# Performance work log

Measured on AMD Instinct MI355X. Metric: run time of the kernel, lower is better.

Reference implementation:

```python
import jax, jax.numpy as jnp
import numpy as np

BIG = 1e9
EPS_BETA = 1e-6
EPS_BN = 1e-5

N_NODES = 50000
N_EDGES = 800000
IN_DIM = 128
OUT_DIM = 128


def setup_inputs() -> dict:
    key = jax.random.key(0)
    ks = jax.random.split(key, 8)
    h = jax.random.normal(ks[0], (N_NODES, IN_DIM), dtype=jnp.float32)
    src = jax.random.randint(ks[1], (N_EDGES,), 0, N_NODES, dtype=jnp.int32)
    dst = jax.random.randint(ks[2], (N_EDGES,), 0, N_NODES, dtype=jnp.int32)
    sigma_GD = jax.random.uniform(ks[3], (N_EDGES,), dtype=jnp.float32)
    fc_w = jax.random.normal(ks[4], (IN_DIM, OUT_DIM), dtype=jnp.float32) / np.sqrt(IN_DIM)
    fc_b = jax.random.normal(ks[5], (OUT_DIM,), dtype=jnp.float32) * 0.01
    attn_w = jax.random.normal(ks[6], (2 * OUT_DIM, 1), dtype=jnp.float32) / np.sqrt(2 * OUT_DIM)
    attn_b = jax.random.normal(ks[7], (1,), dtype=jnp.float32) * 0.01
    bn_gamma = jnp.ones((OUT_DIM,), dtype=jnp.float32)
    bn_beta = jnp.zeros((OUT_DIM,), dtype=jnp.float32)
    return {"h": h, "src": src, "dst": dst, "sigma_GD": sigma_GD,
            "fc_w": fc_w, "fc_b": fc_b, "attn_w": attn_w, "attn_b": attn_b,
            "bn_gamma": bn_gamma, "bn_beta": bn_beta}


def reference(h, src, dst, sigma_GD, fc_w, fc_b, attn_w, attn_b, bn_gamma, bn_beta):
    n = h.shape[0]
    # node projection
    z = h @ fc_w + fc_b                                   # [N, D]
    z = jnp.where(jnp.isinf(z), BIG, z)
    # per-edge attention logits: concat(src,dst) @ W == src@W1 + dst@W2 (avoid concat materialization)
    d = z.shape[1]
    w_src, w_dst = attn_w[:d], attn_w[d:]
    z_src = z[src]                                        # [E, D]
    a = z_src @ w_src + z[dst] @ w_dst + attn_b           # [E, 1]
    a = jnp.where(jnp.isinf(a), BIG, a)
    e = jax.nn.leaky_relu(a, negative_slope=0.01)[:, 0]   # [E]
    # segment softmax over incoming edges (mailbox softmax)
    m = jax.ops.segment_max(e, dst, num_segments=n)       # [N]
    ex = jnp.exp(e - m[dst])
    denom = jax.ops.segment_sum(ex, dst, num_segments=n)  # [N]
    alpha = ex / denom[dst]                               # [E]
    # beta: sigma_GD normalized per destination node
    bsum = jax.ops.segment_sum(sigma_GD, dst, num_segments=n)
    beta = sigma_GD / (bsum[dst] + EPS_BETA)              # [E]
    # weighted scatter-sum of source features
    h_new = jax.ops.segment_sum((alpha * beta)[:, None] * z_src, dst, num_segments=n)  # [N, D]
    h_new = jnp.where(jnp.isinf(h_new), BIG, h_new)
    # BatchNorm1d (training-mode batch stats, biased variance, as torch does)
    mu = h_new.mean(axis=0)
    var = ((h_new - mu) ** 2).mean(axis=0)
    h_bn = (h_new - mu) * jax.lax.rsqrt(var + EPS_BN) * bn_gamma + bn_beta
    return jax.nn.elu(h_bn)
```

## Files before the change

kernel.cpp:

```cpp
#include <hip/hip_runtime.h>
#include <hip/hip_fp16.h>
#include <math.h>

#define N_NODES 50000
#define N_EDGES 800000
#define BIGV 1000000000.0f
#define NBLK_SCAN 196
#define NBLK_GEMM 3125

typedef _Float16 half8 __attribute__((ext_vector_type(8)));
typedef float floatx4 __attribute__((ext_vector_type(4)));

__device__ __forceinline__ float clampinf(float x) { return isinf(x) ? BIGV : x; }

__device__ __forceinline__ void barrier_lgkm_only() {
    __builtin_amdgcn_sched_barrier(0);
    asm volatile("s_waitcnt lgkmcnt(0)" ::: "memory");
    __builtin_amdgcn_s_barrier();
    __builtin_amdgcn_sched_barrier(0);
}

__global__ __launch_bounds__(256) void k_wcast(const float* __restrict__ W,
                                               __half* __restrict__ wt,
                                               int* __restrict__ cursor,
                                               float* __restrict__ bns)
{
    int idx = blockIdx.x * 256 + threadIdx.x;
    int n = idx >> 7, k = idx & 127;
    wt[idx] = __float2half(W[k * 128 + n]);
    for (int i = idx; i < N_NODES; i += 16384) cursor[i] = 0;
    if (idx < 256) bns[idx] = 0.f;
}

__global__ __launch_bounds__(256) void k_gemm(
    const float* __restrict__ h, const __half* __restrict__ wt,
    const float* __restrict__ bias, const float* __restrict__ attn_w,
    const int* __restrict__ dst, __half* __restrict__ zh,
    float* __restrict__ sv, float* __restrict__ tv,
    int* __restrict__ cursor, int* __restrict__ rank)
{
    __shared__ _Float16 hA[16][136];
    __shared__ float spart[4][16], tpart[4][16];

    const int tid = threadIdx.x;
    const int lane = tid & 63;
    const int wv = tid >> 6;
    const int l16 = lane & 15;
    const int oct = lane >> 4;
    const int n0 = wv << 5;
    const int node0 = blockIdx.x << 4;

    const int e = blockIdx.x * 256 + tid;
    const int d = dst[e];

    {
        const float4* h4 = (const float4*)(h + (size_t)node0 * 128);
        for (int i = tid; i < 512; i += 256) {
            int r = i >> 5, c4 = i & 31;
            float4 v = h4[i];
            union { __half2 h2[2]; uint2 u; } pk;
            pk.h2[0] = __floats2half2_rn(v.x, v.y);
            pk.h2[1] = __floats2half2_rn(v.z, v.w);
            *(uint2*)&hA[r][c4 << 2] = pk.u;
        }
    }

    half8 bfrag[4][2];
    #pragma unroll
    for (int kk = 0; kk < 4; ++kk)
        #pragma unroll
        for (int t = 0; t < 2; ++t)
            bfrag[kk][t] = *(const half8*)(wt + (size_t)(n0 + t * 16 + l16) * 128
                                              + kk * 32 + oct * 8);

    const float bv0 = bias[n0 + l16],         bv1 = bias[n0 + 16 + l16];
    const float ws0 = attn_w[n0 + l16],       ws1 = attn_w[n0 + 16 + l16];
    const float wd0 = attn_w[128 + n0 + l16], wd1 = attn_w[128 + n0 + 16 + l16];

    __builtin_amdgcn_sched_barrier(0);
    const int rk = atomicAdd(&cursor[d], 1);

    barrier_lgkm_only();

    floatx4 acc0 = {0.f, 0.f, 0.f, 0.f};
    floatx4 acc1 = {0.f, 0.f, 0.f, 0.f};
    #pragma unroll
    for (int kk = 0; kk < 4; ++kk) {
        half8 a = *(const half8*)&hA[l16][(kk << 5) + (oct << 3)];
        acc0 = __builtin_amdgcn_mfma_f32_16x16x32_f16(a, bfrag[kk][0], acc0, 0, 0, 0);
        acc1 = __builtin_amdgcn_mfma_f32_16x16x32_f16(a, bfrag[kk][1], acc1, 0, 0, 0);
    }

    float s_acc[4], t_acc[4];
    #pragma unroll
    for (int r = 0; r < 4; ++r) {
        float z0 = clampinf(acc0[r] + bv0);
        float z1 = clampinf(acc1[r] + bv1);
        const int row = (oct << 2) + r;
        zh[(size_t)(node0 + row) * 128 + n0 + l16]      = __float2half(z0);
        zh[(size_t)(node0 + row) * 128 + n0 + 16 + l16] = __float2half(z1);
        s_acc[r] = z0 * ws0 + z1 * ws1;
        t_acc[r] = z0 * wd0 + z1 * wd1;
    }
    #pragma unroll
    for (int r = 0; r < 4; ++r) {
        #pragma unroll
        for (int o = 1; o < 16; o <<= 1) {
            s_acc[r] += __shfl_xor(s_acc[r], o);
            t_acc[r] += __shfl_xor(t_acc[r], o);
        }
    }
    if (l16 == 0) {
        #pragma unroll
        for (int r = 0; r < 4; ++r) {
            spart[wv][(oct << 2) + r] = s_acc[r];
            tpart[wv][(oct << 2) + r] = t_acc[r];
        }
    }
    barrier_lgkm_only();
    if (tid < 16) {
        sv[node0 + tid] = spart[0][tid] + spart[1][tid] + spart[2][tid] + spart[3][tid];
        tv[node0 + tid] = tpart[0][tid] + tpart[1][tid] + tpart[2][tid] + tpart[3][tid];
    }
    rank[e] = rk;
}

__global__ __launch_bounds__(256) void k_scan_bsum(const int* __restrict__ cursor,
                                                   int* __restrict__ bsum)
{
    __shared__ int s[256];
    const int t = threadIdx.x;
    const int idx = blockIdx.x * 256 + t;
    s[t] = (idx < N_NODES) ? cursor[idx] : 0;
    __syncthreads();
    for (int off = 128; off; off >>= 1) {
        if (t < off) s[t] += s[t + off];
        __syncthreads();
    }
    if (t == 0) bsum[blockIdx.x] = s[0];
}

__global__ __launch_bounds__(256) void k_scan_final(const int* __restrict__ bsum,
                                                    const int* __restrict__ cursor_in,
                                                    int* __restrict__ colptr)
{
    __shared__ int rs[256];
    __shared__ int s[256];
    const int t = threadIdx.x;

    int rv = (t < NBLK_SCAN) ? bsum[t] : 0;
    rs[t] = rv;
    __syncthreads();
    for (int off = 1; off < 256; off <<= 1) {
        int u = (t >= off) ? rs[t - off] : 0;
        __syncthreads();
        rs[t] += u;
        __syncthreads();
    }
    const int broot = (blockIdx.x > 0) ? rs[blockIdx.x - 1] : 0;
    if (blockIdx.x == 0 && t == 255) colptr[N_NODES] = rs[255];

    const int idx = blockIdx.x * 256 + t;
    int v = (idx < N_NODES) ? cursor_in[idx] : 0;
    s[t] = v;
    __syncthreads();
    for (int off = 1; off < 256; off <<= 1) {
        int u = (t >= off) ? s[t - off] : 0;
        __syncthreads();
        s[t] += u;
        __syncthreads();
    }
    if (idx < N_NODES) colptr[idx] = broot + s[t] - v;
}

__global__ void k_scatter(const int* __restrict__ src, const int* __restrict__ dst,
                          const float* __restrict__ sigma,
                          const int* __restrict__ rank, const int* __restrict__ colptr,
                          const float* __restrict__ sv, const float* __restrict__ tv,
                          const float* __restrict__ attn_b,
                          float4* __restrict__ recs)
{
    int e = blockIdx.x * 256 + threadIdx.x;
    if (e < N_EDGES) {
        int s = src[e];
        int d = dst[e];
        float a = sv[s] + tv[d] + attn_b[0];
        a = clampinf(a);
        float ev = a > 0.f ? a : 0.01f * a;
        int pos = colptr[d] + rank[e];
        float4 rec;
        rec.x = __int_as_float(s);
        rec.y = sigma[e];
        rec.z = ev;
        rec.w = 0.f;
        recs[pos] = rec;
    }
}

__global__ __launch_bounds__(256) void k_agg(
    const int* __restrict__ colptr, const float4* __restrict__ recs,
    const __half* __restrict__ zh, float* __restrict__ out)
{
    const int lane = threadIdx.x & 63;
    const int node = blockIdx.x * 4 + (threadIdx.x >> 6);
    if (node >= N_NODES) return;
    const int base = colptr[node];
    const int deg = colptr[node + 1] - base;

    const int grp = lane >> 4;
    const int l16 = lane & 15;
    float acc[8] = {0.f, 0.f, 0.f, 0.f, 0.f, 0.f, 0.f, 0.f};

    if (deg > 0) {
        if (deg <= 64) {
            int sidx = 0; float sig = 0.f, e = -INFINITY;
            if (lane < deg) {
                float4 r = recs[base + lane];
                sidx = __float_as_int(r.x); sig = r.y; e = r.z;
            }
            float m = e;
            for (int o = 32; o; o >>= 1) m = fmaxf(m, __shfl_xor(m, o));
            float p = (lane < deg) ? __expf(e - m) : 0.f;
            float dn = p, bs = sig;
            for (int o = 32; o; o >>= 1) {
                dn += __shfl_xor(dn, o);
                bs += __shfl_xor(bs, o);
            }
            const float coef = p * sig * (1.0f / dn) / (bs + 1e-6f);
            for (int c = 0; c < deg; c += 4) {
                const int j = c + grp;
                const int js = (j < deg) ? j : 0;
                float cf = __shfl(coef, js);
                int sj = __shfl(sidx, js);
                if (j < deg) {
                    uint4 raw = *(const uint4*)(zh + ((size_t)sj << 7) + (l16 << 3));
                    const __half2* hp = (const __half2*)&raw;
                    #pragma unroll
                    for (int k = 0; k < 4; ++k) {
                        float2 f = __half22float2(hp[k]);
                        acc[2*k]   = fmaf(cf, f.x, acc[2*k]);
                        acc[2*k+1] = fmaf(cf, f.y, acc[2*k+1]);
                    }
                }
            }
        } else {
            float m = -INFINITY;
            for (int i = lane; i < deg; i += 64) m = fmaxf(m, recs[base + i].z);
            for (int o = 32; o; o >>= 1) m = fmaxf(m, __shfl_xor(m, o));
            float dn = 0.f, bs = 0.f;
            for (int i = lane; i < deg; i += 64) {
                float4 r = recs[base + i];
                dn += __expf(r.z - m); bs += r.y;
            }
            for (int o = 32; o; o >>= 1) {
                dn += __shfl_xor(dn, o);
                bs += __shfl_xor(bs, o);
            }
            const float scale = (1.0f / dn) / (bs + 1e-6f);
            for (int c = 0; c < deg; c += 64) {
                int i = c + lane;
                int sidx = 0; float coef = 0.f;
                if (i < deg) {
                    float4 r = recs[base + i];
                    sidx = __float_as_int(r.x);
                    coef = __expf(r.z - m) * r.y * scale;
                }
                const int cnt = min(64, deg - c);
                for (int j = 0; j < cnt; j += 4) {
                    const int jj = j + grp;
                    const int js = (jj < cnt) ? jj : 0;
                    float cf = __shfl(coef, js);
                    int sj = __shfl(sidx, js);
                    if (jj < cnt) {
                        uint4 raw = *(const uint4*)(zh + ((size_t)sj << 7) + (l16 << 3));
                        const __half2* hp = (const __half2*)&raw;
                        #pragma unroll
                        for (int k = 0; k < 4; ++k) {
                            float2 f = __half22float2(hp[k]);
                            acc[2*k]   = fmaf(cf, f.x, acc[2*k]);
                            acc[2*k+1] = fmaf(cf, f.y, acc[2*k+1]);
                        }
                    }
                }
            }
        }
    }
    #pragma unroll
    for (int k = 0; k < 8; ++k) {
        acc[k] += __shfl_xor(acc[k], 16);
        acc[k] += __shfl_xor(acc[k], 32);
    }
    if (grp == 0) {
        float4 o0, o1;
        o0.x = clampinf(acc[0]); o0.y = clampinf(acc[1]);
        o0.z = clampinf(acc[2]); o0.w = clampinf(acc[3]);
        o1.x = clampinf(acc[4]); o1.y = clampinf(acc[5]);
        o1.z = clampinf(acc[6]); o1.w = clampinf(acc[7]);
        float4* op = (float4*)(out + (size_t)node * 128 + (l16 << 3));
        op[0] = o0; op[1] = o1;
    }
}

__global__ __launch_bounds__(256) void k_bnstats(const float* __restrict__ hnew,
                                                 float* __restrict__ sums)
{
    const int tid = threadIdx.x;
    const int f4 = (tid & 31) << 2;
    const int rgrp = tid >> 5;
    float4 s = {0.f, 0.f, 0.f, 0.f}, q = {0.f, 0.f, 0.f, 0.f};
    for (int node = blockIdx.x * 8 + rgrp; node < N_NODES; node += 256 * 8) {
        float4 v = *(const float4*)(hnew + (size_t)node * 128 + f4);
        s.x += v.x; s.y += v.y; s.z += v.z; s.w += v.w;
        q.x += v.x * v.x; q.y += v.y * v.y; q.z += v.z * v.z; q.w += v.w * v.w;
    }
    __shared__ float4 ls[256], lq[256];
    ls[tid] = s; lq[tid] = q;
    __syncthreads();
    for (int off = 128; off >= 32; off >>= 1) {
        if (tid < off) {
            float4 a = ls[tid + off], b = lq[tid + off];
            ls[tid].x += a.x; ls[tid].y += a.y; ls[tid].z += a.z; ls[tid].w += a.w;
            lq[tid].x += b.x; lq[tid].y += b.y; lq[tid].z += b.z; lq[tid].w += b.w;
        }
        __syncthreads();
    }
    if (tid < 32) {
        float4 fs = ls[tid], fq = lq[tid];
        atomicAdd(&sums[f4 + 0], fs.x);
        atomicAdd(&sums[f4 + 1], fs.y);
        atomicAdd(&sums[f4 + 2], fs.z);
        atomicAdd(&sums[f4 + 3], fs.w);
        atomicAdd(&sums[128 + f4 + 0], fq.x);
        atomicAdd(&sums[128 + f4 + 1], fq.y);
        atomicAdd(&sums[128 + f4 + 2], fq.z);
        atomicAdd(&sums[128 + f4 + 3], fq.w);
    }
}

__global__ __launch_bounds__(256) void k_bnapply(float* __restrict__ io,
                                                 const float* __restrict__ sums,
                                                 const float* __restrict__ gamma,
                                                 const float* __restrict__ beta)
{
    __shared__ float sc[128], sh[128];
    const int tid = threadIdx.x;
    if (tid < 128) {
        const float invn = 1.0f / (float)N_NODES;
        float mu = sums[tid] * invn;
        float var = fmaxf(sums[128 + tid] * invn - mu * mu, 0.f);
        float g = gamma[tid] * rsqrtf(var + 1e-5f);
        sc[tid] = g;
        sh[tid] = beta[tid] - mu * g;
    }
    __syncthreads();
    const size_t idx = (size_t)blockIdx.x * 256 + tid;
    const int f4 = ((int)idx & 31) << 2;
    float4 x = ((const float4*)io)[idx];
    float y0 = x.x * sc[f4 + 0] + sh[f4 + 0];
    float y1 = x.y * sc[f4 + 1] + sh[f4 + 1];
    float y2 = x.z * sc[f4 + 2] + sh[f4 + 2];
    float y3 = x.w * sc[f4 + 3] + sh[f4 + 3];
    float4 o;
    o.x = y0 > 0.f ? y0 : expm1f(y0);
    o.y = y1 > 0.f ? y1 : expm1f(y1);
    o.z = y2 > 0.f ? y2 : expm1f(y2);
    o.w = y3 > 0.f ? y3 : expm1f(y3);
    ((float4*)io)[idx] = o;
}

extern "C" void kernel_launch(void* const* d_in, const int* in_sizes, int n_in,
                              void* d_out, int out_size, void* d_ws, size_t ws_size,
                              hipStream_t stream)
{
    const float* h      = (const float*)d_in[0];
    const int*   src    = (const int*)  d_in[1];
    const int*   dst    = (const int*)  d_in[2];
    const float* sigma  = (const float*)d_in[3];
    const float* fc_w   = (const float*)d_in[4];
    const float* fc_b   = (const float*)d_in[5];
    const float* attn_w = (const float*)d_in[6];
    const float* attn_b = (const float*)d_in[7];
    const float* gamma  = (const float*)d_in[8];
    const float* beta   = (const float*)d_in[9];
    float* out = (float*)d_out;

    float4* recs   = (float4*)d_ws;
    __half* zh     = (__half*)(recs + N_EDGES);
    float*  sv     = (float*)(zh + (size_t)N_NODES * 128);
    float*  tv     = sv + N_NODES;
    float*  bns    = tv + N_NODES;
    int*    colptr = (int*)(bns + 256);
    int*    cursor = colptr + 50004;
    int*    bsum   = cursor + N_NODES;
    int*    broot  = bsum + 256;
    __half* wt     = (__half*)(broot + 256);
    int*    rank   = (int*)(wt + 128 * 128);

    k_wcast     <<<64, 256, 0, stream>>>(fc_w, wt, cursor, bns);
    k_gemm      <<<NBLK_GEMM, 256, 0, stream>>>(h, wt, fc_b, attn_w, dst,
                                                zh, sv, tv, cursor, rank);
    k_scan_bsum <<<NBLK_SCAN, 256, 0, stream>>>(cursor, bsum);
    k_scan_final<<<NBLK_SCAN, 256, 0, stream>>>(bsum, cursor, colptr);
    k_scatter   <<<N_EDGES / 256, 256, 0, stream>>>(src, dst, sigma, rank, colptr,
                                                    sv, tv, attn_b, recs);
    k_agg       <<<N_NODES / 4, 256, 0, stream>>>(colptr, recs, zh, out);
    k_bnstats   <<<256, 256, 0, stream>>>(out, bns);
    k_bnapply   <<<(N_NODES * 128) / (256 * 4), 256, 0, stream>>>(out, bns, gamma, beta);
}
```

Measured before the change: 231.4 us.

## Shard per-destination edge counters across eight slots to cut atomic contention

Result: no change. 232.9 us (+0.7%).

```diff
diff --git a/kernel.cpp b/kernel.cpp
--- a/kernel.cpp
+++ b/kernel.cpp
@@ -22,13 +22,15 @@
 
 __global__ __launch_bounds__(256) void k_wcast(const float* __restrict__ W,
                                                __half* __restrict__ wt,
-                                               int* __restrict__ cursor,
+                                               int* __restrict__ cnt,
                                                float* __restrict__ bns)
 {
     int idx = blockIdx.x * 256 + threadIdx.x;
     int n = idx >> 7, k = idx & 127;
     wt[idx] = __float2half(W[k * 128 + n]);
-    for (int i = idx; i < N_NODES; i += 16384) cursor[i] = 0;
+    uint4 z; z.x = 0u; z.y = 0u; z.z = 0u; z.w = 0u;
+    uint4* c4 = (uint4*)cnt;
+    for (int i = idx; i < N_NODES * 4; i += 16384) c4[i] = z;
     if (idx < 256) bns[idx] = 0.f;
 }
 
@@ -37,7 +39,7 @@
     const float* __restrict__ bias, const float* __restrict__ attn_w,
     const int* __restrict__ dst, __half* __restrict__ zh,
     float* __restrict__ sv, float* __restrict__ tv,
-    int* __restrict__ cursor, int* __restrict__ rank)
+    int* __restrict__ cnt, unsigned short* __restrict__ rank)
 {
     __shared__ _Float16 hA[16][136];
     __shared__ float spart[4][16], tpart[4][16];
@@ -52,6 +54,7 @@
 
     const int e = blockIdx.x * 256 + tid;
     const int d = dst[e];
+    const int shard = blockIdx.x & 7;
 
     {
         const float4* h4 = (const float4*)(h + (size_t)node0 * 128);
@@ -78,7 +81,7 @@
     const float wd0 = attn_w[128 + n0 + l16], wd1 = attn_w[128 + n0 + 16 + l16];
 
     __builtin_amdgcn_sched_barrier(0);
-    const int rk = atomicAdd(&cursor[d], 1);
+    const int rk = atomicAdd(&cnt[(d << 4) + shard], 1);
 
     barrier_lgkm_only();
 
@@ -122,26 +125,45 @@
         sv[node0 + tid] = spart[0][tid] + spart[1][tid] + spart[2][tid] + spart[3][tid];
         tv[node0 + tid] = tpart[0][tid] + tpart[1][tid] + tpart[2][tid] + tpart[3][tid];
     }
-    rank[e] = rk;
-}
-
-__global__ __launch_bounds__(256) void k_scan_bsum(const int* __restrict__ cursor,
+    rank[e] = (unsigned short)rk;
+}
+
+__global__ __launch_bounds__(256) void k_scan_bsum(int* __restrict__ cnt,
+                                                   int* __restrict__ deg,
                                                    int* __restrict__ bsum)
 {
-    __shared__ int s[256];
+    __shared__ int sdeg[256];
     const int t = threadIdx.x;
     const int idx = blockIdx.x * 256 + t;
-    s[t] = (idx < N_NODES) ? cursor[idx] : 0;
+    int dsum = 0;
+    if (idx < N_NODES) {
+        uint4* p = (uint4*)(cnt + ((size_t)idx << 4));
+        uint4 a = p[0], b = p[1];
+        unsigned e0 = 0;
+        unsigned e1 = e0 + a.x;
+        unsigned e2 = e1 + a.y;
+        unsigned e3 = e2 + a.z;
+        unsigned e4 = e3 + a.w;
+        unsigned e5 = e4 + b.x;
+        unsigned e6 = e5 + b.y;
+        unsigned e7 = e6 + b.z;
+        dsum = (int)(e7 + b.w);
+        uint4 pa; pa.x = e0; pa.y = e1; pa.z = e2; pa.w = e3;
+        uint4 pb; pb.x = e4; pb.y = e5; pb.z = e6; pb.w = e7;
+        p[0] = pa; p[1] = pb;
+        deg[idx] = dsum;
+    }
+    sdeg[t] = dsum;
     __syncthreads();
     for (int off = 128; off; off >>= 1) {
-        if (t < off) s[t] += s[t + off];
-        __syncthreads();
-    }
-    if (t == 0) bsum[blockIdx.x] = s[0];
+        if (t < off) sdeg[t] += sdeg[t + off];
+        __syncthreads();
+    }
+    if (t == 0) bsum[blockIdx.x] = sdeg[0];
 }
 
 __global__ __launch_bounds__(256) void k_scan_final(const int* __restrict__ bsum,
-                                                    const int* __restrict__ cursor_in,
+                                                    const int* __restrict__ deg,
                                                     int* __restrict__ colptr)
 {
     __shared__ int rs[256];
@@ -161,7 +183,7 @@
     if (blockIdx.x == 0 && t == 255) colptr[N_NODES] = rs[255];
 
     const int idx = blockIdx.x * 256 + t;
-    int v = (idx < N_NODES) ? cursor_in[idx] : 0;
+    int v = (idx < N_NODES) ? deg[idx] : 0;
     s[t] = v;
     __syncthreads();
     for (int off = 1; off < 256; off <<= 1) {
@@ -175,7 +197,9 @@
 
 __global__ void k_scatter(const int* __restrict__ src, const int* __restrict__ dst,
                           const float* __restrict__ sigma,
-                          const int* __restrict__ rank, const int* __restrict__ colptr,
+                          const unsigned short* __restrict__ rank,
+                          const int* __restrict__ colptr,
+                          const int* __restrict__ cnt,
                           const float* __restrict__ sv, const float* __restrict__ tv,
                           const float* __restrict__ attn_b,
                           float4* __restrict__ recs)
@@ -184,10 +208,11 @@
     if (e < N_EDGES) {
         int s = src[e];
         int d = dst[e];
+        int shard = (e >> 8) & 7;
         float a = sv[s] + tv[d] + attn_b[0];
         a = clampinf(a);
         float ev = a > 0.f ? a : 0.01f * a;
-        int pos = colptr[d] + rank[e];
+        int pos = colptr[d] + cnt[(d << 4) + shard] + (int)rank[e];
         float4 rec;
         rec.x = __int_as_float(s);
         rec.y = sigma[e];
@@ -265,13 +290,13 @@
                     sidx = __float_as_int(r.x);
                     coef = __expf(r.z - m) * r.y * scale;
                 }
-                const int cnt = min(64, deg - c);
-                for (int j = 0; j < cnt; j += 4) {
+                const int cnt2 = min(64, deg - c);
+                for (int j = 0; j < cnt2; j += 4) {
                     const int jj = j + grp;
-                    const int js = (jj < cnt) ? jj : 0;
+                    const int js = (jj < cnt2) ? jj : 0;
                     float cf = __shfl(coef, js);
                     int sj = __shfl(sidx, js);
-                    if (jj < cnt) {
+                    if (jj < cnt2) {
                         uint4 raw = *(const uint4*)(zh + ((size_t)sj << 7) + (l16 << 3));
                         const __half2* hp = (const __half2*)&raw;
                         #pragma unroll
@@ -390,19 +415,20 @@
     float*  tv     = sv + N_NODES;
     float*  bns    = tv + N_NODES;
     int*    colptr = (int*)(bns + 256);
-    int*    cursor = colptr + 50004;
-    int*    bsum   = cursor + N_NODES;
+    int*    deg    = colptr + 50004;
+    int*    bsum   = deg + N_NODES;
     int*    broot  = bsum + 256;
     __half* wt     = (__half*)(broot + 256);
-    int*    rank   = (int*)(wt + 128 * 128);
-
-    k_wcast     <<<64, 256, 0, stream>>>(fc_w, wt, cursor, bns);
+    unsigned short* rank = (unsigned short*)(wt + 128 * 128);
+    int*    cnt    = (int*)(rank + N_EDGES);
+
+    k_wcast     <<<64, 256, 0, stream>>>(fc_w, wt, cnt, bns);
     k_gemm      <<<NBLK_GEMM, 256, 0, stream>>>(h, wt, fc_b, attn_w, dst,
-                                                zh, sv, tv, cursor, rank);
-    k_scan_bsum <<<NBLK_SCAN, 256, 0, stream>>>(cursor, bsum);
-    k_scan_final<<<NBLK_SCAN, 256, 0, stream>>>(bsum, cursor, colptr);
+                                                zh, sv, tv, cnt, rank);
+    k_scan_bsum <<<NBLK_SCAN, 256, 0, stream>>>(cnt, deg, bsum);
+    k_scan_final<<<NBLK_SCAN, 256, 0, stream>>>(bsum, deg, colptr);
     k_scatter   <<<N_EDGES / 256, 256, 0, stream>>>(src, dst, sigma, rank, colptr,
-                                                    sv, tv, attn_b, recs);
+                                                    cnt, sv, tv, attn_b, recs);
     k_agg       <<<N_NODES / 4, 256, 0, stream>>>(colptr, recs, zh, out);
     k_bnstats   <<<256, 256, 0, stream>>>(out, bns);
     k_bnapply   <<<(N_NODES * 128) / (256 * 4), 256, 0, stream>>>(out, bns, gamma, beta);
```

## Replace global-atomic CSR build with two-pass shared-memory bucket sort by destination

Applied to the files above, without the earlier changes.

Result: slower. 251.6 us (+8.7%).

```diff
diff --git a/kernel.cpp b/kernel.cpp
--- a/kernel.cpp
+++ b/kernel.cpp
@@ -5,8 +5,10 @@
 #define N_NODES 50000
 #define N_EDGES 800000
 #define BIGV 1000000000.0f
-#define NBLK_SCAN 196
 #define NBLK_GEMM 3125
+#define CHUNK 4096
+#define NBLK_A 196
+#define NBUCKET 196
 
 typedef _Float16 half8 __attribute__((ext_vector_type(8)));
 typedef float floatx4 __attribute__((ext_vector_type(4)));
@@ -20,24 +22,35 @@
     __builtin_amdgcn_sched_barrier(0);
 }
 
-__global__ __launch_bounds__(256) void k_wcast(const float* __restrict__ W,
-                                               __half* __restrict__ wt,
-                                               int* __restrict__ cursor,
-                                               float* __restrict__ bns)
-{
-    int idx = blockIdx.x * 256 + threadIdx.x;
-    int n = idx >> 7, k = idx & 127;
-    wt[idx] = __float2half(W[k * 128 + n]);
-    for (int i = idx; i < N_NODES; i += 16384) cursor[i] = 0;
+__global__ __launch_bounds__(256) void k_prep(const float* __restrict__ W,
+                                              __half* __restrict__ wt,
+                                              float* __restrict__ bns,
+                                              const int* __restrict__ dst,
+                                              int* __restrict__ counts)
+{
+    __shared__ int hist[NBUCKET];
+    const int t = threadIdx.x;
+    const int idx = blockIdx.x * 256 + t;
+    if (idx < 16384) {
+        int n = idx >> 7, k = idx & 127;
+        wt[idx] = __float2half(W[k * 128 + n]);
+    }
     if (idx < 256) bns[idx] = 0.f;
+    if (t < NBUCKET) hist[t] = 0;
+    __syncthreads();
+    const int base = blockIdx.x * CHUNK;
+    for (int i = t; i < CHUNK; i += 256) {
+        int e = base + i;
+        if (e < N_EDGES) atomicAdd(&hist[dst[e] >> 8], 1);
+    }
+    __syncthreads();
+    if (t < NBUCKET) counts[blockIdx.x * NBUCKET + t] = hist[t];
 }
 
 __global__ __launch_bounds__(256) void k_gemm(
     const float* __restrict__ h, const __half* __restrict__ wt,
     const float* __restrict__ bias, const float* __restrict__ attn_w,
-    const int* __restrict__ dst, __half* __restrict__ zh,
-    float* __restrict__ sv, float* __restrict__ tv,
-    int* __restrict__ cursor, int* __restrict__ rank)
+    __half* __restrict__ zh, float* __restrict__ sv, float* __restrict__ tv)
 {
     __shared__ _Float16 hA[16][136];
     __shared__ float spart[4][16], tpart[4][16];
@@ -49,9 +62,6 @@
     const int oct = lane >> 4;
     const int n0 = wv << 5;
     const int node0 = blockIdx.x << 4;
-
-    const int e = blockIdx.x * 256 + tid;
-    const int d = dst[e];
 
     {
         const float4* h4 = (const float4*)(h + (size_t)node0 * 128);
@@ -76,9 +86,6 @@
     const float bv0 = bias[n0 + l16],         bv1 = bias[n0 + 16 + l16];
     const float ws0 = attn_w[n0 + l16],       ws1 = attn_w[n0 + 16 + l16];
     const float wd0 = attn_w[128 + n0 + l16], wd1 = attn_w[128 + n0 + 16 + l16];
-
-    __builtin_amdgcn_sched_barrier(0);
-    const int rk = atomicAdd(&cursor[d], 1);
 
     barrier_lgkm_only();
 
@@ -122,72 +129,95 @@
         sv[node0 + tid] = spart[0][tid] + spart[1][tid] + spart[2][tid] + spart[3][tid];
         tv[node0 + tid] = tpart[0][tid] + tpart[1][tid] + tpart[2][tid] + tpart[3][tid];
     }
-    rank[e] = rk;
-}
-
-__global__ __launch_bounds__(256) void k_scan_bsum(const int* __restrict__ cursor,
-                                                   int* __restrict__ bsum)
-{
-    __shared__ int s[256];
+}
+
+__global__ __launch_bounds__(256) void k_scatterA(const int* __restrict__ dst,
+                                                  const int* __restrict__ counts,
+                                                  int* __restrict__ tmp,
+                                                  int* __restrict__ bbase_g)
+{
+    __shared__ int cur[NBUCKET];
+    __shared__ int stot[256];
     const int t = threadIdx.x;
-    const int idx = blockIdx.x * 256 + t;
-    s[t] = (idx < N_NODES) ? cursor[idx] : 0;
-    __syncthreads();
-    for (int off = 128; off; off >>= 1) {
-        if (t < off) s[t] += s[t + off];
+    const int self = blockIdx.x;
+    int pre = 0, tot = 0;
+    if (t < NBUCKET) {
+        for (int b = 0; b < NBLK_A; ++b) {
+            int c = counts[b * NBUCKET + t];
+            if (b < self) pre += c;
+            tot += c;
+        }
+    }
+    stot[t] = (t < NBUCKET) ? tot : 0;
+    __syncthreads();
+    for (int off = 1; off < 256; off <<= 1) {
+        int u = (t >= off) ? stot[t - off] : 0;
         __syncthreads();
-    }
-    if (t == 0) bsum[blockIdx.x] = s[0];
-}
-
-__global__ __launch_bounds__(256) void k_scan_final(const int* __restrict__ bsum,
-                                                    const int* __restrict__ cursor_in,
-                                                    int* __restrict__ colptr)
-{
-    __shared__ int rs[256];
-    __shared__ int s[256];
+        stot[t] += u;
+        __syncthreads();
+    }
+    if (t < NBUCKET) {
+        const int bb = stot[t] - tot;
+        cur[t] = bb + pre;
+        if (self == 0) bbase_g[t] = bb;
+    }
+    if (self == 0 && t == 0) bbase_g[NBUCKET] = N_EDGES;
+    __syncthreads();
+    const int base = self * CHUNK;
+    for (int i = t; i < CHUNK; i += 256) {
+        int e = base + i;
+        if (e < N_EDGES) {
+            int pos = atomicAdd(&cur[dst[e] >> 8], 1);
+            tmp[pos] = e;
+        }
+    }
+}
+
+__global__ __launch_bounds__(256) void k_binB(
+    const int* __restrict__ tmp, const int* __restrict__ bbase_g,
+    const int* __restrict__ dst, const int* __restrict__ src,
+    const float* __restrict__ sigma,
+    const float* __restrict__ sv, const float* __restrict__ tv,
+    const float* __restrict__ attn_b,
+    int* __restrict__ colptr, float4* __restrict__ recs)
+{
+    __shared__ int hist[256];
+    __shared__ int scn[256];
+    __shared__ int cur[256];
     const int t = threadIdx.x;
-
-    int rv = (t < NBLK_SCAN) ? bsum[t] : 0;
-    rs[t] = rv;
+    const int b = blockIdx.x;
+    const int s0 = bbase_g[b];
+    const int n = bbase_g[b + 1] - s0;
+    hist[t] = 0;
+    __syncthreads();
+    for (int i = t; i < n; i += 256) {
+        int e = tmp[s0 + i];
+        atomicAdd(&hist[dst[e] & 255], 1);
+    }
+    __syncthreads();
+    scn[t] = hist[t];
     __syncthreads();
     for (int off = 1; off < 256; off <<= 1) {
-        int u = (t >= off) ? rs[t - off] : 0;
+        int u = (t >= off) ? scn[t - off] : 0;
         __syncthreads();
-        rs[t] += u;
+        scn[t] += u;
         __syncthreads();
     }
-    const int broot = (blockIdx.x > 0) ? rs[blockIdx.x - 1] : 0;
-    if (blockIdx.x == 0 && t == 255) colptr[N_NODES] = rs[255];
-
-    const int idx = blockIdx.x * 256 + t;
-    int v = (idx < N_NODES) ? cursor_in[idx] : 0;
-    s[t] = v;
-    __syncthreads();
-    for (int off = 1; off < 256; off <<= 1) {
-        int u = (t >= off) ? s[t - off] : 0;
-        __syncthreads();
-        s[t] += u;
-        __syncthreads();
-    }
-    if (idx < N_NODES) colptr[idx] = broot + s[t] - v;
-}
-
-__global__ void k_scatter(const int* __restrict__ src, const int* __restrict__ dst,
-                          const float* __restrict__ sigma,
-                          const int* __restrict__ rank, const int* __restrict__ colptr,
-                          const float* __restrict__ sv, const float* __restrict__ tv,
-                          const float* __restrict__ attn_b,
-                          float4* __restrict__ recs)
-{
-    int e = blockIdx.x * 256 + threadIdx.x;
-    if (e < N_EDGES) {
+    const int excl = scn[t] - hist[t];
+    cur[t] = s0 + excl;
+    const int node = (b << 8) + t;
+    if (node < N_NODES) colptr[node] = s0 + excl;
+    if (b == 0 && t == 0) colptr[N_NODES] = N_EDGES;
+    __syncthreads();
+    const float ab = attn_b[0];
+    for (int i = t; i < n; i += 256) {
+        int e = tmp[s0 + i];
+        int d = dst[e];
+        int pos = atomicAdd(&cur[d & 255], 1);
         int s = src[e];
-        int d = dst[e];
-        float a = sv[s] + tv[d] + attn_b[0];
+        float a = sv[s] + tv[d] + ab;
         a = clampinf(a);
         float ev = a > 0.f ? a : 0.01f * a;
-        int pos = colptr[d] + rank[e];
         float4 rec;
         rec.x = __int_as_float(s);
         rec.y = sigma[e];
@@ -265,13 +295,13 @@
                     sidx = __float_as_int(r.x);
                     coef = __expf(r.z - m) * r.y * scale;
                 }
-                const int cnt = min(64, deg - c);
-                for (int j = 0; j < cnt; j += 4) {
+                const int cnt2 = min(64, deg - c);
+                for (int j = 0; j < cnt2; j += 4) {
                     const int jj = j + grp;
-                    const int js = (jj < cnt) ? jj : 0;
+                    const int js = (jj < cnt2) ? jj : 0;
                     float cf = __shfl(coef, js);
                     int sj = __shfl(sidx, js);
-                    if (jj < cnt) {
+                    if (jj < cnt2) {
                         uint4 raw = *(const uint4*)(zh + ((size_t)sj << 7) + (l16 << 3));
                         const __half2* hp = (const __half2*)&raw;
                         #pragma unroll
@@ -390,20 +420,17 @@
     float*  tv     = sv + N_NODES;
     float*  bns    = tv + N_NODES;
     int*    colptr = (int*)(bns + 256);
-    int*    cursor = colptr + 50004;
-    int*    bsum   = cursor + N_NODES;
-    int*    broot  = bsum + 256;
-    __half* wt     = (__half*)(broot + 256);
-    int*    rank   = (int*)(wt + 128 * 128);
-
-    k_wcast     <<<64, 256, 0, stream>>>(fc_w, wt, cursor, bns);
-    k_gemm      <<<NBLK_GEMM, 256, 0, stream>>>(h, wt, fc_b, attn_w, dst,
-                                                zh, sv, tv, cursor, rank);
-    k_scan_bsum <<<NBLK_SCAN, 256, 0, stream>>>(cursor, bsum);
-    k_scan_final<<<NBLK_SCAN, 256, 0, stream>>>(bsum, cursor, colptr);
-    k_scatter   <<<N_EDGES / 256, 256, 0, stream>>>(src, dst, sigma, rank, colptr,
-                                                    sv, tv, attn_b, recs);
-    k_agg       <<<N_NODES / 4, 256, 0, stream>>>(colptr, recs, zh, out);
-    k_bnstats   <<<256, 256, 0, stream>>>(out, bns);
-    k_bnapply   <<<(N_NODES * 128) / (256 * 4), 256, 0, stream>>>(out, bns, gamma, beta);
-}
+    __half* wt     = (__half*)(colptr + 50004);
+    int*    counts = (int*)(wt + 128 * 128);
+    int*    bbase  = counts + 38416;
+    int*    tmp    = bbase + 256;
+
+    k_prep     <<<NBLK_A, 256, 0, stream>>>(fc_w, wt, bns, dst, counts);
+    k_scatterA <<<NBLK_A, 256, 0, stream>>>(dst, counts, tmp, bbase);
+    k_gemm     <<<NBLK_GEMM, 256, 0, stream>>>(h, wt, fc_b, attn_w, zh, sv, tv);
+    k_binB     <<<NBUCKET, 256, 0, stream>>>(tmp, bbase, dst, src, sigma,
+                                             sv, tv, attn_b, colptr, recs);
+    k_agg      <<<N_NODES / 4, 256, 0, stream>>>(colptr, recs, zh, out);
+    k_bnstats  <<<256, 256, 0, stream>>>(out, bns);
+    k_bnapply  <<<(N_NODES * 128) / (256 * 4), 256, 0, stream>>>(out, bns, gamma, beta);
+}
```
